# Kernel optimization log

Hardware: AMD Instinct MI355X
Metric: run time of the kernel (lower is better)

Reference implementation:

```python
import jax, jax.numpy as jnp
import numpy as np

B, CIN, H, W = 16, 3, 112, 112
S, D, C, NC = 3, 4, 128, 100   # num_scales, depth, channels, num_classes
THRESH = 0.9
WSCALE = 0.05  # keep activations numerically sane through relu-conv cascade


def _conv3x3(x, w, b):
    # x: [B,Cin,H,W], w: [Cout,Cin,3,3]
    y = jax.lax.conv_general_dilated(
        x, w, window_strides=(1, 1), padding='SAME',
        dimension_numbers=('NCHW', 'OIHW', 'NCHW'))
    return y + b[None, :, None, None]


def setup_inputs() -> dict:
    key = jax.random.key(0)
    k = jax.random.split(key, 7)
    return {
        'x': jax.random.normal(k[0], (B, CIN, H, W), jnp.float32),
        'init_w': jax.random.normal(k[1], (S, C, CIN, 3, 3), jnp.float32) * WSCALE,
        'init_b': jax.random.normal(k[2], (S, C), jnp.float32) * WSCALE,
        'block_w': jax.random.normal(k[3], (D, S, C, C, 3, 3), jnp.float32) * WSCALE,
        'block_b': jax.random.normal(k[4], (D, S, C), jnp.float32) * WSCALE,
        'cls_w': jax.random.normal(k[5], (D, NC, C), jnp.float32) * WSCALE,
        'cls_b': jax.random.normal(k[6], (D, NC), jnp.float32) * WSCALE,
    }


def reference(x, init_w, init_b, block_w, block_b, cls_w, cls_b):
    # init blocks: one conv per scale (no activation, as in source)
    feats = [_conv3x3(x, init_w[s], init_b[s]) for s in range(S)]

    outputs = jnp.zeros((x.shape[0], cls_w.shape[1]), x.dtype)
    exited = jnp.zeros((x.shape[0],), jnp.bool_)

    # exit_layers = [0..D-1], so classifier index == block index
    for i in range(D):
        feats = [jax.nn.relu(_conv3x3(feats[s], block_w[i, s], block_b[i, s]))
                 for s in range(S)]
        pooled = feats[-1].mean(axis=(2, 3))              # [B, C]
        logits = pooled @ cls_w[i].T + cls_b[i]           # [B, NC]
        conf = jnp.max(jax.nn.softmax(logits, axis=-1), axis=-1)
        take = jnp.logical_and(~exited, conf >= THRESH)   # vectorized early-exit
        outputs = jnp.where(take[:, None], logits, outputs)
        exited = jnp.logical_or(exited, take)

    # samples that never exited get the last classifier's logits
    final_logits = feats[-1].mean(axis=(2, 3)) @ cls_w[-1].T + cls_b[-1]
    outputs = jnp.where(exited[:, None], outputs, final_logits)
    return outputs
```

## Files before the change

kernel.cpp:

```cpp
#include <hip/hip_runtime.h>
#include <hip/hip_bf16.h>


typedef unsigned int uint;
typedef unsigned short u16;
typedef __bf16 bf16x8 __attribute__((ext_vector_type(8)));
typedef short short8 __attribute__((ext_vector_type(8)));
typedef unsigned short ushort8 __attribute__((ext_vector_type(8)));
typedef float f32x4 __attribute__((ext_vector_type(4)));

#define NB   16
#define CCH  128
#define NCLS 100
#define HW   12544
#define NTILE 98

__device__ __forceinline__ u16 f2bf(float f) {
    uint u = __float_as_uint(f);
    return (u16)((u + 0x7fffu + ((u >> 16) & 1u)) >> 16);
}

__global__ __launch_bounds__(256) void convert_w(
    const float* __restrict__ bw, u16* __restrict__ wb)
{
    int idx = blockIdx.x * 256 + threadIdx.x;
    if (idx >= 4 * 9 * 16384) return;
    int d = idx / 147456, r = idx % 147456;
    int t = r / 16384, r2 = r & 16383;
    int co = r2 >> 7, ci = r2 & 127;
    float v = bw[((size_t)(d * 3 + 2) * 16384 + co * 128 + ci) * 9 + t];
    wb[idx] = f2bf(v);
}

__global__ __launch_bounds__(256) void conv_init(
    const float* __restrict__ in,
    const float* __restrict__ wgt,
    const float* __restrict__ bias,
    u16* __restrict__ outp)
{
    const int tile = blockIdx.x;
    const int cg   = blockIdx.y;
    const int n    = blockIdx.z;
    const int h0 = (tile / 7) * 16, w0 = (tile % 7) * 16;
    const int tid = threadIdx.x;
    const int sid = tid & 63, wv = tid >> 6;
    const int tx = sid & 7, ty = sid >> 3;

    __shared__ float s_in[3][18][18];
    __shared__ float s_w[3][9][32];

    float acc[2][2][8];
    #pragma unroll
    for (int a = 0; a < 2; a++)
        #pragma unroll
        for (int b = 0; b < 2; b++)
            #pragma unroll
            for (int c = 0; c < 8; c++) acc[a][b][c] = 0.f;

    const float* in_n = in + (size_t)n * 3 * HW;
    const int cbase = cg * 32;

    for (int e = tid; e < 3 * 324; e += 256) {
        int ck = e / 324, p = e % 324;
        int y = p / 18, x = p % 18;
        int gh = h0 + y - 1, gw = w0 + x - 1;
        float v = 0.f;
        if ((unsigned)gh < 112u && (unsigned)gw < 112u)
            v = in_n[(size_t)ck * HW + gh * 112 + gw];
        s_in[ck][y][x] = v;
    }
    for (int e = tid; e < 3 * 9 * 32; e += 256) {
        int co = e / 27, r = e % 27;
        int ck = r / 9, kidx = r % 9;
        s_w[ck][kidx][co] = wgt[((size_t)(cbase + co) * 3 + ck) * 9 + kidx];
    }
    __syncthreads();

    #pragma unroll
    for (int ck = 0; ck < 3; ck++) {
        float rowv[4][4];
        #pragma unroll
        for (int r = 0; r < 4; r++) {
            float2 a  = *(const float2*)&s_in[ck][ty * 2 + r][tx * 2];
            float2 b2 = *(const float2*)&s_in[ck][ty * 2 + r][tx * 2 + 2];
            rowv[r][0] = a.x; rowv[r][1] = a.y;
            rowv[r][2] = b2.x; rowv[r][3] = b2.y;
        }
        #pragma unroll
        for (int kh = 0; kh < 3; kh++)
            #pragma unroll
            for (int kw = 0; kw < 3; kw++) {
                float i00 = rowv[kh][kw],     i01 = rowv[kh][kw + 1];
                float i10 = rowv[kh + 1][kw], i11 = rowv[kh + 1][kw + 1];
                const float* wp = &s_w[ck][kh * 3 + kw][wv * 8];
                #pragma unroll
                for (int co = 0; co < 8; co++) {
                    float wval = wp[co];
                    acc[0][0][co] += i00 * wval;
                    acc[0][1][co] += i01 * wval;
                    acc[1][0][co] += i10 * wval;
                    acc[1][1][co] += i11 * wval;
                }
            }
    }

    float bv[8];
    #pragma unroll
    for (int co = 0; co < 8; co++) bv[co] = bias[cbase + wv * 8 + co];
    #pragma unroll
    for (int dy = 0; dy < 2; dy++)
        #pragma unroll
        for (int dx = 0; dx < 2; dx++) {
            ushort8 pk;
            #pragma unroll
            for (int co = 0; co < 8; co++)
                pk[co] = f2bf(acc[dy][dx][co] + bv[co]);
            int h = h0 + ty * 2 + dy, w = w0 + tx * 2 + dx;
            *(ushort8*)(outp + (((size_t)n * HW + h * 112 + w) << 7) + cbase + wv * 8) = pk;
        }
}

#define AS 40
#define W_S 40

template<bool STORE>
__global__ __launch_bounds__(256, 3) void conv_mfma(
    const u16* __restrict__ in,
    const u16* __restrict__ wb,
    const float* __restrict__ bias,
    u16* __restrict__ outp,
    float* __restrict__ partial)
{
    __shared__ u16 s_in[180 * AS];
    __shared__ u16 s_w[2 * 128 * W_S];
    float* s_pool = (float*)s_in;

    const int tile = blockIdx.x;
    const int n    = blockIdx.y;
    const int h0 = (tile / 7) * 8, w0 = (tile % 7) * 16;
    const int tid = threadIdx.x, lane = tid & 63;
    const int wid = tid >> 6, wm = wid >> 1, wn = wid & 1;
    const int l15 = lane & 15, l4 = lane >> 4;

    const u16* in_n = in + ((size_t)n * HW << 7);

    int st_px[3], st_c8[3];
    long st_src[3];
    #pragma unroll
    for (int r = 0; r < 3; ++r) {
        int g = tid + (r << 8);
        int px = g >> 2, c8 = (g & 3) << 3;
        int hh = px / 18, ww = px - hh * 18;
        int gh = h0 + hh - 1, gw = w0 + ww - 1;
        bool inb = (g < 720) && ((unsigned)gh < 112u) && ((unsigned)gw < 112u);
        st_px[r] = (g < 720) ? px : -1;
        st_c8[r] = c8;
        st_src[r] = inb ? (((long)(gh * 112 + gw)) << 7) + c8 : -1;
    }

    const int co0 = tid >> 2, k0 = (tid & 3) << 3;

    #pragma unroll
    for (int r = 0; r < 3; ++r) {
        if (st_px[r] >= 0) {
            uint4 v = make_uint4(0, 0, 0, 0);
            if (st_src[r] >= 0) v = *(const uint4*)(in_n + st_src[r]);
            *(uint4*)(s_in + st_px[r] * AS + st_c8[r]) = v;
        }
    }
    *(uint4*)(s_w + co0 * W_S + k0)        = *(const uint4*)(wb + (co0 << 7) + k0);
    *(uint4*)(s_w + (co0 + 64) * W_S + k0) = *(const uint4*)(wb + ((co0 + 64) << 7) + k0);

    uint4 wcur0, wcur1, wnxt0, wnxt1;
    {
        const u16* ws1 = wb + 16384;
        wcur0 = *(const uint4*)(ws1 + (co0 << 7) + k0);
        wcur1 = *(const uint4*)(ws1 + ((co0 + 64) << 7) + k0);
    }

    f32x4 acc[4][4];
    #pragma unroll
    for (int i = 0; i < 4; ++i)
        #pragma unroll
        for (int j = 0; j < 4; ++j)
            #pragma unroll
            for (int e = 0; e < 4; ++e) acc[i][j][e] = 0.f;

    int a_base[4], b_base[4];
    #pragma unroll
    for (int fi = 0; fi < 4; ++fi) a_base[fi] = (wm * 4 + fi) * 18 + l15;
    #pragma unroll
    for (int nj = 0; nj < 4; ++nj) b_base[nj] = (wn * 64 + nj * 16 + l15) * W_S + (l4 << 3);

    __syncthreads();

    for (int q = 0; q < 4; ++q) {
        if (q > 0) {
            #pragma unroll
            for (int r = 0; r < 3; ++r) {
                if (st_px[r] >= 0) {
                    uint4 v = make_uint4(0, 0, 0, 0);
                    if (st_src[r] >= 0)
                        v = *(const uint4*)(in_n + st_src[r] + (q << 5));
                    *(uint4*)(s_in + st_px[r] * AS + st_c8[r]) = v;
                }
            }
            __syncthreads();
        }

        #pragma unroll
        for (int t = 0; t < 9; ++t) {
            const int s = q * 9 + t;
            const int kh = t / 3, kw = t - kh * 3;

            bf16x8 a[4], b[4];
            #pragma unroll
            for (int fi = 0; fi < 4; ++fi) {
                const u16* p = s_in + (a_base[fi] + kh * 18 + kw) * AS + (l4 << 3);
                a[fi] = __builtin_bit_cast(bf16x8, *(const short8*)p);
            }
            const u16* wbuf = s_w + (s & 1) * (128 * W_S);
            #pragma unroll
            for (int nj = 0; nj < 4; ++nj)
                b[nj] = __builtin_bit_cast(bf16x8, *(const short8*)(wbuf + b_base[nj]));

            {
                int sp = s + 2; if (sp >= 36) sp -= 36;
                const u16* wsj = wb + (sp % 9) * 16384 + ((sp / 9) << 5);
                wnxt0 = *(const uint4*)(wsj + (co0 << 7) + k0);
                wnxt1 = *(const uint4*)(wsj + ((co0 + 64) << 7) + k0);
            }

            #pragma unroll
            for (int fi = 0; fi < 4; ++fi)
                #pragma unroll
                for (int nj = 0; nj < 4; ++nj)
                    acc[fi][nj] = __builtin_amdgcn_mfma_f32_16x16x32_bf16(
                        a[fi], b[nj], acc[fi][nj], 0, 0, 0);

            {
                u16* wdst = s_w + ((s + 1) & 1) * (128 * W_S);
                *(uint4*)(wdst + co0 * W_S + k0)        = wcur0;
                *(uint4*)(wdst + (co0 + 64) * W_S + k0) = wcur1;
            }
            wcur0 = wnxt0; wcur1 = wnxt1;

            asm volatile("s_waitcnt lgkmcnt(0)" ::: "memory");
            __builtin_amdgcn_s_barrier();
            __builtin_amdgcn_sched_barrier(0);
        }
    }

    float bv[4], ps[4];
    #pragma unroll
    for (int nj = 0; nj < 4; ++nj) { bv[nj] = bias[wn * 64 + nj * 16 + l15]; ps[nj] = 0.f; }
    u16* out_n = outp + ((size_t)n * HW << 7);
    #pragma unroll
    for (int fi = 0; fi < 4; ++fi) {
        int h = h0 + wm * 4 + fi;
        #pragma unroll
        for (int j = 0; j < 4; ++j) {
            int w = w0 + (l4 << 2) + j;
            u16* pr = out_n + ((size_t)(h * 112 + w) << 7);
            #pragma unroll
            for (int nj = 0; nj < 4; ++nj) {
                float v = fmaxf(acc[fi][nj][j] + bv[nj], 0.f);
                ps[nj] += v;
                if (STORE) pr[wn * 64 + nj * 16 + l15] = f2bf(v);
            }
        }
    }
    #pragma unroll
    for (int nj = 0; nj < 4; ++nj) {
        ps[nj] += __shfl_xor(ps[nj], 16, 64);
        ps[nj] += __shfl_xor(ps[nj], 32, 64);
    }
    __syncthreads();
    if (l4 == 0) {
        #pragma unroll
        for (int nj = 0; nj < 4; ++nj)
            s_pool[wm * 128 + wn * 64 + nj * 16 + l15] = ps[nj];
    }
    __syncthreads();
    if (tid < 128)
        partial[((size_t)n * NTILE + tile) * 128 + tid] = s_pool[tid] + s_pool[128 + tid];
}

__global__ __launch_bounds__(128) void logits_k(
    const float* __restrict__ partial,
    const float* __restrict__ cw,
    const float* __restrict__ cb,
    float* __restrict__ lg)
{
    const int i = blockIdx.x, n = blockIdx.y;
    const int tid = threadIdx.x;
    __shared__ float pool[128];
    const float* pp = partial + ((size_t)(i * NB + n) * NTILE) * 128;
    float s = 0.f;
    for (int t = 0; t < NTILE; ++t) s += pp[t * 128 + tid];
    pool[tid] = s * (1.f / HW);
    __syncthreads();
    if (tid < NCLS) {
        const float* wp = cw + ((size_t)i * NCLS + tid) * CCH;
        float a = cb[i * NCLS + tid];
        #pragma unroll
        for (int c = 0; c < CCH; c += 4) {
            float4 w4 = *(const float4*)(wp + c);
            a += pool[c] * w4.x + pool[c + 1] * w4.y
               + pool[c + 2] * w4.z + pool[c + 3] * w4.w;
        }
        lg[(i * NB + n) * NCLS + tid] = a;
    }
}

__global__ __launch_bounds__(256) void select_k(
    const float* __restrict__ lg,
    float* __restrict__ out)
{
    __shared__ float slg[4 * NB * NCLS];
    __shared__ int chosen[NB];
    const int tid = threadIdx.x;
    for (int e = tid; e < 4 * NB * NCLS; e += 256) slg[e] = lg[e];
    __syncthreads();
    if (tid < NB) {
        int n = tid, ch = 3;
        for (int i = 0; i < 3; i++) {
            const float* row = &slg[(i * NB + n) * NCLS];
            float m = -1e30f;
            for (int j = 0; j < NCLS; j++) m = fmaxf(m, row[j]);
            float se = 0.f;
            for (int j = 0; j < NCLS; j++) se += expf(row[j] - m);
            if (1.f / se >= 0.9f) { ch = i; break; }
        }
        chosen[n] = ch;
    }
    __syncthreads();
    for (int e = tid; e < NB * NCLS; e += 256) {
        int n = e / NCLS, j = e % NCLS;
        out[e] = slg[(chosen[n] * NB + n) * NCLS + j];
    }
}

extern "C" void kernel_launch(void* const* d_in, const int* in_sizes, int n_in,
                              void* d_out, int out_size, void* d_ws, size_t ws_size,
                              hipStream_t stream) {
    const float* x       = (const float*)d_in[0];
    const float* init_w  = (const float*)d_in[1];
    const float* init_b  = (const float*)d_in[2];
    const float* block_w = (const float*)d_in[3];
    const float* block_b = (const float*)d_in[4];
    const float* cls_w   = (const float*)d_in[5];
    const float* cls_b   = (const float*)d_in[6];
    float* out = (float*)d_out;

    char* ws = (char*)d_ws;
    u16* fA        = (u16*)ws;
    u16* fB        = (u16*)(ws + 51380224);
    u16* wb        = (u16*)(ws + 102760448);
    float* partial = (float*)(ws + 103940096);
    float* lgbuf   = (float*)(ws + 107151360);

    convert_w<<<2304, 256, 0, stream>>>(block_w, wb);
    conv_init<<<dim3(49, 4, NB), 256, 0, stream>>>(
        x, init_w + 2 * 128 * 27, init_b + 2 * 128, fA);

    u16* cur = fA;
    u16* nxt = fB;
    for (int i = 0; i < 4; ++i) {
        if (i < 3)
            conv_mfma<true><<<dim3(NTILE, NB), 256, 0, stream>>>(
                cur, wb + (size_t)i * 147456, block_b + (i * 3 + 2) * 128, nxt,
                partial + (size_t)i * NB * NTILE * 128);
        else
            conv_mfma<false><<<dim3(NTILE, NB), 256, 0, stream>>>(
                cur, wb + (size_t)i * 147456, block_b + (i * 3 + 2) * 128, nxt,
                partial + (size_t)i * NB * NTILE * 128);
        u16* t = cur; cur = nxt; nxt = t;
    }

    logits_k<<<dim3(4, NB), 128, 0, stream>>>(partial, cls_w, cls_b, lgbuf);
    select_k<<<1, 256, 0, stream>>>(lgbuf, out);
}
```

Measured before the change: 339.3 us.

## Quad-buffer conv weights with XOR swizzle and one barrier per two taps

Weight staging in LDS grows from double to quadruple buffering with a two-step-ahead register prefetch, so a single barrier covers two MFMA tap steps instead of one. Weight tiles drop row padding in favour of an XOR swizzle to avoid bank conflicts, and the outer loop is fully unrolled into paired steps with input-channel reloads placed at the chunk boundaries. The aim is to halve barrier count and shrink LDS padding, at the cost of more registers, code size and trickier synchronisation.

```diff
diff --git a/kernel.cpp b/kernel.cpp
--- a/kernel.cpp
+++ b/kernel.cpp
@@ -121,7 +121,6 @@
 }
 
 #define AS 40
-#define W_S 40
 
 template<bool STORE>
 __global__ __launch_bounds__(256, 3) void conv_mfma(
@@ -132,7 +131,7 @@
     float* __restrict__ partial)
 {
     __shared__ u16 s_in[180 * AS];
-    __shared__ u16 s_w[2 * 128 * W_S];
+    __shared__ u16 s_w[4][128 * 32];
     float* s_pool = (float*)s_in;
 
     const int tile = blockIdx.x;
@@ -144,38 +143,41 @@
 
     const u16* in_n = in + ((size_t)n * HW << 7);
 
-    int st_px[3], st_c8[3];
-    long st_src[3];
-    #pragma unroll
-    for (int r = 0; r < 3; ++r) {
-        int g = tid + (r << 8);
-        int px = g >> 2, c8 = (g & 3) << 3;
-        int hh = px / 18, ww = px - hh * 18;
-        int gh = h0 + hh - 1, gw = w0 + ww - 1;
-        bool inb = (g < 720) && ((unsigned)gh < 112u) && ((unsigned)gw < 112u);
-        st_px[r] = (g < 720) ? px : -1;
-        st_c8[r] = c8;
-        st_src[r] = inb ? (((long)(gh * 112 + gw)) << 7) + c8 : -1;
-    }
-
-    const int co0 = tid >> 2, k0 = (tid & 3) << 3;
-
-    #pragma unroll
-    for (int r = 0; r < 3; ++r) {
-        if (st_px[r] >= 0) {
+    const int co0 = tid >> 2;
+    const int g0  = (tid & 3) ^ ((tid >> 3) & 3);
+    const int k0  = g0 << 3;
+    const int wp0 = (tid & 3) << 3;
+
+    #pragma unroll
+    for (int s01 = 0; s01 < 2; ++s01) {
+        const u16* src = wb + s01 * 16384;
+        uint4 va = *(const uint4*)(src + (co0 << 7) + k0);
+        uint4 vb = *(const uint4*)(src + ((co0 + 64) << 7) + k0);
+        *(uint4*)(&s_w[s01][co0 * 32] + wp0) = va;
+        *(uint4*)(&s_w[s01][(co0 + 64) * 32] + wp0) = vb;
+    }
+    uint4 wA0, wA1, wB0, wB1;
+    {
+        const u16* s2 = wb + 2 * 16384;
+        const u16* s3 = wb + 3 * 16384;
+        wA0 = *(const uint4*)(s2 + (co0 << 7) + k0);
+        wA1 = *(const uint4*)(s2 + ((co0 + 64) << 7) + k0);
+        wB0 = *(const uint4*)(s3 + (co0 << 7) + k0);
+        wB1 = *(const uint4*)(s3 + ((co0 + 64) << 7) + k0);
+    }
+
+    #pragma unroll
+    for (int r2 = 0; r2 < 3; ++r2) {
+        int g = tid + (r2 << 8);
+        if (g < 720) {
+            int px = g >> 2, c8 = (g & 3) << 3;
+            int hh = px / 18, ww2 = px - hh * 18;
+            int gh = h0 + hh - 1, gw = w0 + ww2 - 1;
             uint4 v = make_uint4(0, 0, 0, 0);
-            if (st_src[r] >= 0) v = *(const uint4*)(in_n + st_src[r]);
-            *(uint4*)(s_in + st_px[r] * AS + st_c8[r]) = v;
-        }
-    }
-    *(uint4*)(s_w + co0 * W_S + k0)        = *(const uint4*)(wb + (co0 << 7) + k0);
-    *(uint4*)(s_w + (co0 + 64) * W_S + k0) = *(const uint4*)(wb + ((co0 + 64) << 7) + k0);
-
-    uint4 wcur0, wcur1, wnxt0, wnxt1;
-    {
-        const u16* ws1 = wb + 16384;
-        wcur0 = *(const uint4*)(ws1 + (co0 << 7) + k0);
-        wcur1 = *(const uint4*)(ws1 + ((co0 + 64) << 7) + k0);
+            if ((unsigned)gh < 112u && (unsigned)gw < 112u)
+                v = *(const uint4*)(in_n + ((size_t)(gh * 112 + gw) << 7) + c8);
+            *(uint4*)(s_in + px * AS + c8) = v;
+        }
     }
 
     f32x4 acc[4][4];
@@ -190,45 +192,33 @@
     #pragma unroll
     for (int fi = 0; fi < 4; ++fi) a_base[fi] = (wm * 4 + fi) * 18 + l15;
     #pragma unroll
-    for (int nj = 0; nj < 4; ++nj) b_base[nj] = (wn * 64 + nj * 16 + l15) * W_S + (l4 << 3);
-
-    __syncthreads();
-
-    for (int q = 0; q < 4; ++q) {
-        if (q > 0) {
-            #pragma unroll
-            for (int r = 0; r < 3; ++r) {
-                if (st_px[r] >= 0) {
-                    uint4 v = make_uint4(0, 0, 0, 0);
-                    if (st_src[r] >= 0)
-                        v = *(const uint4*)(in_n + st_src[r] + (q << 5));
-                    *(uint4*)(s_in + st_px[r] * AS + st_c8[r]) = v;
-                }
-            }
-            __syncthreads();
-        }
-
-        #pragma unroll
-        for (int t = 0; t < 9; ++t) {
-            const int s = q * 9 + t;
-            const int kh = t / 3, kw = t - kh * 3;
-
+    for (int nj = 0; nj < 4; ++nj)
+        b_base[nj] = (wn * 64 + nj * 16 + l15) * 32 + ((l4 ^ ((l15 >> 1) & 3)) << 3);
+
+    __syncthreads();
+
+    #pragma unroll
+    for (int P = 0; P < 18; ++P) {
+        const int s0 = 2 * P, s1 = 2 * P + 1;
+
+        {
+            const int t = s0 % 9, kh = t / 3, kw = t - kh * 3;
             bf16x8 a[4], b[4];
             #pragma unroll
             for (int fi = 0; fi < 4; ++fi) {
                 const u16* p = s_in + (a_base[fi] + kh * 18 + kw) * AS + (l4 << 3);
                 a[fi] = __builtin_bit_cast(bf16x8, *(const short8*)p);
             }
-            const u16* wbuf = s_w + (s & 1) * (128 * W_S);
+            const u16* rb = &s_w[s0 & 3][0];
             #pragma unroll
             for (int nj = 0; nj < 4; ++nj)
-                b[nj] = __builtin_bit_cast(bf16x8, *(const short8*)(wbuf + b_base[nj]));
-
-            {
-                int sp = s + 2; if (sp >= 36) sp -= 36;
-                const u16* wsj = wb + (sp % 9) * 16384 + ((sp / 9) << 5);
-                wnxt0 = *(const uint4*)(wsj + (co0 << 7) + k0);
-                wnxt1 = *(const uint4*)(wsj + ((co0 + 64) << 7) + k0);
+                b[nj] = __builtin_bit_cast(bf16x8, *(const short8*)(rb + b_base[nj]));
+
+            uint4 nA0, nA1;
+            if (s0 + 4 < 36) {
+                const u16* srcn = wb + ((s0 + 4) % 9) * 16384 + ((s0 + 4) / 9) * 32;
+                nA0 = *(const uint4*)(srcn + (co0 << 7) + k0);
+                nA1 = *(const uint4*)(srcn + ((co0 + 64) << 7) + k0);
             }
 
             #pragma unroll
@@ -238,13 +228,92 @@
                     acc[fi][nj] = __builtin_amdgcn_mfma_f32_16x16x32_bf16(
                         a[fi], b[nj], acc[fi][nj], 0, 0, 0);
 
-            {
-                u16* wdst = s_w + ((s + 1) & 1) * (128 * W_S);
-                *(uint4*)(wdst + co0 * W_S + k0)        = wcur0;
-                *(uint4*)(wdst + (co0 + 64) * W_S + k0) = wcur1;
-            }
-            wcur0 = wnxt0; wcur1 = wnxt1;
-
+            if (s0 + 2 < 36) {
+                u16* wd = &s_w[(s0 + 2) & 3][0];
+                *(uint4*)(wd + co0 * 32 + wp0) = wA0;
+                *(uint4*)(wd + (co0 + 64) * 32 + wp0) = wA1;
+            }
+            if (s0 + 4 < 36) { wA0 = nA0; wA1 = nA1; }
+        }
+
+        if (s0 % 9 == 8) {
+            const int qn = s0 / 9 + 1;
+            asm volatile("s_waitcnt lgkmcnt(0)" ::: "memory");
+            __builtin_amdgcn_s_barrier();
+            #pragma unroll
+            for (int r2 = 0; r2 < 3; ++r2) {
+                int g = tid + (r2 << 8);
+                if (g < 720) {
+                    int px = g >> 2, c8 = (g & 3) << 3;
+                    int hh = px / 18, ww2 = px - hh * 18;
+                    int gh = h0 + hh - 1, gw = w0 + ww2 - 1;
+                    uint4 v = make_uint4(0, 0, 0, 0);
+                    if ((unsigned)gh < 112u && (unsigned)gw < 112u)
+                        v = *(const uint4*)(in_n + ((size_t)(gh * 112 + gw) << 7)
+                                            + (qn << 5) + c8);
+                    *(uint4*)(s_in + px * AS + c8) = v;
+                }
+            }
+            asm volatile("s_waitcnt lgkmcnt(0)" ::: "memory");
+            __builtin_amdgcn_s_barrier();
+            __builtin_amdgcn_sched_barrier(0);
+        }
+
+        {
+            const int t = s1 % 9, kh = t / 3, kw = t - kh * 3;
+            bf16x8 a[4], b[4];
+            #pragma unroll
+            for (int fi = 0; fi < 4; ++fi) {
+                const u16* p = s_in + (a_base[fi] + kh * 18 + kw) * AS + (l4 << 3);
+                a[fi] = __builtin_bit_cast(bf16x8, *(const short8*)p);
+            }
+            const u16* rb = &s_w[s1 & 3][0];
+            #pragma unroll
+            for (int nj = 0; nj < 4; ++nj)
+                b[nj] = __builtin_bit_cast(bf16x8, *(const short8*)(rb + b_base[nj]));
+
+            uint4 nB0, nB1;
+            if (s1 + 4 < 36) {
+                const u16* srcn = wb + ((s1 + 4) % 9) * 16384 + ((s1 + 4) / 9) * 32;
+                nB0 = *(const uint4*)(srcn + (co0 << 7) + k0);
+                nB1 = *(const uint4*)(srcn + ((co0 + 64) << 7) + k0);
+            }
+
+            #pragma unroll
+            for (int fi = 0; fi < 4; ++fi)
+                #pragma unroll
+                for (int nj = 0; nj < 4; ++nj)
+                    acc[fi][nj] = __builtin_amdgcn_mfma_f32_16x16x32_bf16(
+                        a[fi], b[nj], acc[fi][nj], 0, 0, 0);
+
+            if (s1 + 2 < 36) {
+                u16* wd = &s_w[(s1 + 2) & 3][0];
+                *(uint4*)(wd + co0 * 32 + wp0) = wB0;
+                *(uint4*)(wd + (co0 + 64) * 32 + wp0) = wB1;
+            }
+            if (s1 + 4 < 36) { wB0 = nB0; wB1 = nB1; }
+        }
+
+        asm volatile("s_waitcnt lgkmcnt(0)" ::: "memory");
+        __builtin_amdgcn_s_barrier();
+        __builtin_amdgcn_sched_barrier(0);
+
+        if (s1 % 9 == 8 && s1 != 35) {
+            const int qn = s1 / 9 + 1;
+            #pragma unroll
+            for (int r2 = 0; r2 < 3; ++r2) {
+                int g = tid + (r2 << 8);
+                if (g < 720) {
+                    int px = g >> 2, c8 = (g & 3) << 3;
+                    int hh = px / 18, ww2 = px - hh * 18;
+                    int gh = h0 + hh - 1, gw = w0 + ww2 - 1;
+                    uint4 v = make_uint4(0, 0, 0, 0);
+                    if ((unsigned)gh < 112u && (unsigned)gw < 112u)
+                        v = *(const uint4*)(in_n + ((size_t)(gh * 112 + gw) << 7)
+                                            + (qn << 5) + c8);
+                    *(uint4*)(s_in + px * AS + c8) = v;
+                }
+            }
             asm volatile("s_waitcnt lgkmcnt(0)" ::: "memory");
             __builtin_amdgcn_s_barrier();
             __builtin_amdgcn_sched_barrier(0);
```

After: 327.3 us. 3.5% less time.
